# Kernel tuning notes

Measured on AMD Instinct MI355X. Metric: run time of the kernel, lower is better.

Reference implementation:

```python
import jax, jax.numpy as jnp
import numpy as np

SEARCH_RANGE = 4  # matches init_kwargs


def setup_inputs() -> dict:
    key = jax.random.key(0)
    k1, k2 = jax.random.split(key)
    shape = (8, 256, 64, 128)  # [B, C, H, W]
    feature1 = jax.random.normal(k1, shape, dtype=jnp.float32)
    feature2 = jax.random.normal(k2, shape, dtype=jnp.float32)
    return {"feature1": feature1, "feature2": feature2}


def reference(feature1, feature2):
    R = SEARCH_RANGE
    b, c, h, w = feature1.shape
    # zero-pad feature2 spatially by R on each side
    f2p = jnp.pad(feature2, ((0, 0), (0, 0), (R, R), (R, R)))
    D = 2 * R + 1
    # shift offsets in the same order as the original nested loop (idx outer, jdx inner)
    offsets = jnp.stack(
        jnp.meshgrid(jnp.arange(D), jnp.arange(D), indexing="ij"), axis=-1
    ).reshape(-1, 2)  # [81, 2]

    def corr_one(ij):
        win = jax.lax.dynamic_slice(f2p, (0, 0, ij[0], ij[1]), (b, c, h, w))
        return jnp.sum(feature1 * win, axis=1)  # [B, H, W]

    dots = jax.vmap(corr_one)(offsets)  # [81, B, H, W]
    return jnp.transpose(dots, (1, 0, 2, 3))  # [B, 81, H, W]
```

## Files before the change

kernel.cpp:

```cpp
#include <hip/hip_runtime.h>
#include <cstdint>

typedef __attribute__((ext_vector_type(8))) short short8;
typedef __attribute__((ext_vector_type(4))) float floatx4;
typedef __attribute__((ext_vector_type(2))) unsigned int uintx2;
typedef __attribute__((ext_vector_type(4))) unsigned int uintx4;

__device__ __forceinline__ uint32_t pack2(float a, float b) {
    uint32_t ua = __builtin_bit_cast(uint32_t, a);
    uint32_t ub = __builtin_bit_cast(uint32_t, b);
    ua = (ua + 0x7FFFu + ((ua >> 16) & 1u)) >> 16;
    ub = (ub + 0x7FFFu + ((ub >> 16) & 1u)) >> 16;
    return ua | (ub << 16);
}

#define CC_SLAB  ((size_t)8 * 64 * 2304)
#define T2P_WORDS (8 * CC_SLAB)
#define WS_NEED   (T2P_WORDS * 4 + 4096)

__global__ __launch_bounds__(256)
void transpose_f2(const float* __restrict__ f2, uint32_t* __restrict__ t2p) {
    __shared__ float t[64][33];
    const int tid = threadIdx.x;
    const int bid = blockIdx.x;
    const int b = bid & 7, h = (bid >> 3) & 63, wt = bid >> 9;
    const int w0 = wt * 32;
    const float* f2b = f2 + (size_t)b * 256 * 8192 + (size_t)h * 128 + w0;

    const int rw = tid & 31, rc8 = tid >> 5;
    const int tp = tid & 127, rr = tid >> 7;
    const int m  = tp & 15;

    for (int cc = 0; cc < 4; ++cc) {
        if (cc) __syncthreads();
#pragma unroll
        for (int i = 0; i < 8; ++i)
            t[rc8 * 8 + i][rw] = f2b[(size_t)(cc * 64 + rc8 * 8 + i) * 8192 + rw];
        __syncthreads();
        const int cc2 = 2 * cc + rr;
        uint32_t* dst = t2p + (size_t)cc2 * CC_SLAB
                        + ((size_t)b * 64 + h) * 2304 + (size_t)(w0 + 4) * 16;
#pragma unroll
        for (int i = 0; i < 4; ++i) {
            int d = i * 128 + tp;
            int j = d >> 4;
            dst[d] = pack2(t[rr * 32 + 2 * m][j], t[rr * 32 + 2 * m + 1][j]);
        }
    }
    if (wt == 0) {
        for (int idx = tid; idx < 512; idx += 256) {
            int cc2 = idx >> 6, o = idx & 63;
            t2p[(size_t)cc2 * CC_SLAB + ((size_t)b * 64 + h) * 2304 + o] = 0;
        }
    }
    if (wt == 3) {
        for (int idx = tid; idx < 1536; idx += 256) {
            int cc2 = idx / 192, o = idx % 192;
            t2p[(size_t)cc2 * CC_SLAB + ((size_t)b * 64 + h) * 2304 + 132 * 16 + o] = 0;
        }
    }
    if (bid == 0) {
        uint32_t* z = t2p + T2P_WORDS;
        for (int idx = tid; idx < 1024; idx += 256) z[idx] = 0;
    }
}

#define AS1 __attribute__((address_space(1)))
#define AS3 __attribute__((address_space(3)))

__device__ __forceinline__ void gld_lds16(const uint32_t* src, uint32_t* dst) {
    __builtin_amdgcn_global_load_lds((const AS1 void*)src, (AS3 void*)dst, 16, 0, 0);
}

__global__ __launch_bounds__(512, 3)
void corr2(const float* __restrict__ f1, const uint32_t* __restrict__ t2p,
           const uint32_t* __restrict__ wsZ, float* __restrict__ out) {
    __shared__ uint32_t ldsB[2 * 8192];

    const int tid  = threadIdx.x;
    const int lane = tid & 63;
    const int wh   = tid >> 6;
    const int n15  = lane & 15;
    const int q    = lane >> 4;

    const int bid = blockIdx.x;
    const int b  = bid & 7;
    const int ht = (bid >> 3) & 7;
    const int wt = bid >> 6;
    const int h0 = 8 * ht, w0 = 16 * wt;
    const int h  = h0 + wh;

    const float* f1b = f1 + (size_t)b * 256 * 8192;

    const uint32_t* bbase[4];
    size_t bstep[4];
    int bdst[4];
#pragma unroll
    for (int ki = 0; ki < 4; ++ki) {
        int k = 4 * wh + ki, r = k >> 1, gh = h0 - 4 + r;
        int c = (k & 1) * 16 + (lane >> 2);
        int gd = (lane & 3) ^ ((c >> 1) & 3);
        bool ok = (unsigned)gh < 64u;
        bbase[ki] = ok ? t2p + ((size_t)b * 64 + gh) * 2304 + (size_t)(w0 + c) * 16 + gd * 4
                       : wsZ + lane * 4;
        bstep[ki] = ok ? CC_SLAB : 0;
        bdst[ki]  = k * 256;
    }

    const float* aBase = f1b + (size_t)h * 128 + w0 + n15;

    floatx4 acc[9][2];
#pragma unroll
    for (int di = 0; di < 9; ++di)
#pragma unroll
        for (int t = 0; t < 2; ++t)
            acc[di][t] = (floatx4){0.f, 0.f, 0.f, 0.f};

    const int rdB = n15 * 16 + ((q ^ ((n15 >> 1) & 3)) << 2);

    auto stageB = [&](int bufsel, int cc) {
        uint32_t* dst = ldsB + bufsel * 8192;
#pragma unroll
        for (int ki = 0; ki < 4; ++ki)
            gld_lds16(bbase[ki] + (size_t)cc * bstep[ki], &dst[bdst[ki]]);
    };
    auto loadA = [&](float* r, int cc) {
        const float* ap = aBase + (size_t)(32 * cc + 8 * q) * 8192;
#pragma unroll
        for (int j = 0; j < 8; ++j) r[j] = ap[(size_t)j * 8192];
    };
    auto packA = [&](const float* r) -> short8 {
        uintx4 av = {pack2(r[0], r[1]), pack2(r[2], r[3]),
                     pack2(r[4], r[5]), pack2(r[6], r[7])};
        return __builtin_bit_cast(short8, av);
    };
    auto mfma9 = [&](int bufsel, short8 a0) {
        const uint32_t* bufB = ldsB + bufsel * 8192;
#pragma unroll
        for (int di = 0; di < 9; ++di) {
            const uint32_t* p0 = bufB + (wh + di) * 512 + rdB;
            uintx4 v0 = *(const uintx4*)p0;
            uintx4 v1 = *(const uintx4*)(p0 + 128);
            short8 b0 = __builtin_bit_cast(short8, v0);
            short8 b1 = __builtin_bit_cast(short8, v1);
            acc[di][0] = __builtin_amdgcn_mfma_f32_16x16x32_bf16(a0, b0, acc[di][0], 0, 0, 0);
            acc[di][1] = __builtin_amdgcn_mfma_f32_16x16x32_bf16(a0, b1, acc[di][1], 0, 0, 0);
        }
    };

    float rA0[8], rA1[8];

    stageB(0, 0);
    __builtin_amdgcn_sched_barrier(0);
    loadA(rA0, 0);
    __builtin_amdgcn_sched_barrier(0);
    stageB(1, 1);
    __builtin_amdgcn_sched_barrier(0);
    loadA(rA1, 1);
    __builtin_amdgcn_sched_barrier(0);

#define CHUNK(K, VM, RS)                                                      \
    {                                                                         \
        asm volatile("s_waitcnt vmcnt(" #VM ")\n\ts_barrier" ::: "memory");   \
        if ((K) >= 1 && (K) < 7) stageB(((K) + 1) & 1, (K) + 1);              \
        __builtin_amdgcn_sched_barrier(0);                                    \
        short8 a0 = packA(RS);                                                \
        if ((K) < 6) loadA(RS, (K) + 2);                                      \
        __builtin_amdgcn_sched_barrier(0);                                    \
        mfma9((K) & 1, a0);                                                   \
    }

    CHUNK(0, 20, rA0)
    CHUNK(1, 16, rA1)
    CHUNK(2, 8,  rA0)
    CHUNK(3, 8,  rA1)
    CHUNK(4, 8,  rA0)
    CHUNK(5, 8,  rA1)
    CHUNK(6, 8,  rA0)
    CHUNK(7, 0,  rA1)
#undef CHUNK

    const size_t base = ((size_t)b * 81) * 8192 + (size_t)h * 128 + w0;
#pragma unroll
    for (int di = 0; di < 9; ++di) {
#pragma unroll
        for (int t = 0; t < 2; ++t) {
#pragma unroll
            for (int r = 0; r < 4; ++r) {
                int mp = 4 * q + r;
                int dj = t * 8 + n15 - mp;
                if (dj >= 0 && dj <= 8 && (t == 0 || n15 >= 8)) {
                    out[base + (size_t)(di * 9 + dj) * 8192 + mp] = acc[di][t][r];
                }
            }
        }
    }
}

#define CS 18
#define A_WORDS (8 * 16 * CS)
#define B_ROWS  13
#define B_WORDS (B_ROWS * 24 * CS)

__device__ __forceinline__ short8 frag_ld(const uint32_t* p) {
    uintx2 lo = *(const uintx2*)p;
    uintx2 hi = *(const uintx2*)(p + 2);
    uintx4 v = {lo.x, lo.y, hi.x, hi.y};
    return __builtin_bit_cast(short8, v);
}

__global__ __launch_bounds__(512, 4)
void corr_kernel(const float* __restrict__ f1, const float* __restrict__ f2,
                 float* __restrict__ out) {
    __shared__ uint32_t ldsA[2 * A_WORDS];
    __shared__ uint32_t ldsB2[2 * B_WORDS];

    const int tid  = threadIdx.x;
    const int lane = tid & 63;
    const int wh   = tid >> 6;
    const int n15  = lane & 15;
    const int q    = lane >> 4;

    const int bid    = blockIdx.x;
    const int b      = bid & 7;
    const int dihalf = (bid >> 3) & 1;
    const int ht     = (bid >> 4) & 7;
    const int wt     = bid >> 7;

    const int w0 = wt * 16;
    const int h0 = ht * 8;
    const int h  = h0 + wh;

    const int diN    = dihalf ? 4 : 5;
    const int diBase = dihalf * 5;
    const int ghBase = dihalf ? (h0 + 1) : (h0 - 4);

    const float* f1b = f1 + (size_t)b * 256 * 8192;
    const float* f2b = f2 + (size_t)b * 256 * 8192;

    const int aw4 = tid & 3, akp = (tid >> 2) & 15, arow = tid >> 6;
    int aOffG = (2 * akp) * 8192 + (h0 + arow) * 128 + (w0 + 4 * aw4);
    const int aLds = (arow * 16 + 4 * aw4) * CS + akp;

    int bOffG[3]; int bLds[3]; uint32_t bMask[3];
#pragma unroll
    for (int s = 0; s < 3; ++s) {
        int t = tid + 512 * s;
        int w4 = t % 6;
        int r2 = t / 6;
        int kp = r2 & 15, row = r2 >> 4;
        int gh = ghBase + row;
        int gw = w0 - 4 + 4 * w4;
        bool live = (t < 1152);
        bool inb  = live && ((unsigned)gh < 64u) && ((unsigned)gw < 128u);
        bOffG[s] = inb ? ((2 * kp) * 8192 + gh * 128 + gw) : 0;
        bLds[s]  = live ? ((row * 24 + 4 * w4) * CS + kp) : ((12 * 24 + (tid & 7)) * CS);
        bMask[s] = inb ? 0xFFFFFFFFu : 0u;
    }

    floatx4 acc[5][2];
#pragma unroll
    for (int dl = 0; dl < 5; ++dl)
#pragma unroll
        for (int t = 0; t < 2; ++t)
            acc[dl][t] = (floatx4){0.f, 0.f, 0.f, 0.f};

    floatx4 rA[2], rB[3][2];
    uint32_t pkA[4], pkB[12];

    auto issue = [&]() {
        rA[0] = *(const floatx4*)(f1b + aOffG);
        rA[1] = *(const floatx4*)(f1b + aOffG + 8192);
        aOffG += 32 * 8192;
#pragma unroll
        for (int s = 0; s < 3; ++s) {
            rB[s][0] = *(const floatx4*)(f2b + bOffG[s]);
            rB[s][1] = *(const floatx4*)(f2b + bOffG[s] + 8192);
            bOffG[s] += 32 * 8192;
        }
    };
    auto packall = [&]() {
#pragma unroll
        for (int i = 0; i < 4; ++i) pkA[i] = pack2(rA[0][i], rA[1][i]);
#pragma unroll
        for (int s = 0; s < 3; ++s)
#pragma unroll
            for (int i = 0; i < 4; ++i)
                pkB[4 * s + i] = pack2(rB[s][0][i], rB[s][1][i]) & bMask[s];
    };

    issue(); packall();

    for (int ch = 0; ch < 8; ++ch) {
        uint32_t* bufA = ldsA + (ch & 1) * A_WORDS;
        uint32_t* bufB = ldsB2 + (ch & 1) * B_WORDS;
#pragma unroll
        for (int i = 0; i < 4; ++i) bufA[aLds + i * CS] = pkA[i];
#pragma unroll
        for (int s = 0; s < 3; ++s)
#pragma unroll
            for (int i = 0; i < 4; ++i) bufB[bLds[s] + i * CS] = pkB[4 * s + i];
        if (ch < 7) issue();
        __syncthreads();

        const uint32_t* pa = bufA + (wh * 16 + n15) * CS + 4 * q;
        short8 a0 = frag_ld(pa);
        const uint32_t* pb = bufB + (wh * 24 + n15) * CS + 4 * q;
#pragma unroll
        for (int dl = 0; dl < 5; ++dl) {
            if (dl < diN) {
                const uint32_t* pp = pb + dl * (24 * CS);
                short8 b0 = frag_ld(pp);
                short8 b1 = frag_ld(pp + 8 * CS);
                acc[dl][0] = __builtin_amdgcn_mfma_f32_16x16x32_bf16(a0, b0, acc[dl][0], 0, 0, 0);
                acc[dl][1] = __builtin_amdgcn_mfma_f32_16x16x32_bf16(a0, b1, acc[dl][1], 0, 0, 0);
            }
        }
        if (ch < 7) packall();
    }

    const size_t base = ((size_t)b * 81) * 8192 + (size_t)h * 128 + w0;
#pragma unroll
    for (int dl = 0; dl < 5; ++dl) {
        if (dl < diN) {
            const int dio = diBase + dl;
#pragma unroll
            for (int t = 0; t < 2; ++t) {
#pragma unroll
                for (int r = 0; r < 4; ++r) {
                    int mp = 4 * q + r;
                    int dj = t * 8 + n15 - mp;
                    if (dj >= 0 && dj <= 8 && (t == 0 || n15 >= 8)) {
                        out[base + (size_t)(dio * 9 + dj) * 8192 + mp] = acc[dl][t][r];
                    }
                }
            }
        }
    }
}

extern "C" void kernel_launch(void* const* d_in, const int* in_sizes, int n_in,
                              void* d_out, int out_size, void* d_ws, size_t ws_size,
                              hipStream_t stream) {
    const float* f1 = (const float*)d_in[0];
    const float* f2 = (const float*)d_in[1];
    float* out = (float*)d_out;
    if (ws_size >= WS_NEED && d_ws != nullptr) {
        uint32_t* t2p = (uint32_t*)d_ws;
        transpose_f2<<<dim3(2048), dim3(256), 0, stream>>>(f2, t2p);
        corr2<<<dim3(512), dim3(512), 0, stream>>>(f1, t2p, t2p + T2P_WORDS, out);
    } else {
        corr_kernel<<<dim3(1024), dim3(512), 0, stream>>>(f1, f2, out);
    }
}
```

Measured before the change: 177.3 us.

## Enlarge correlation tile to 16 rows with 1024-thread blocks and 4-stage B pipeline

The correlation kernel now uses 1024-thread blocks covering 16 output rows instead of 8, so each staged feature2 halo (24 rows) serves twice as many rows and less halo is reloaded. B staging grows from double to quadruple buffering, with dummy lanes dumping into a scratch LDS area. The channel-chunk order is rotated per block to spread memory traffic. The trade-off is fewer blocks (256), higher LDS use and a less uniform load mapping, which may reduce occupancy and latency hiding.

```diff
diff --git a/kernel.cpp b/kernel.cpp
--- a/kernel.cpp
+++ b/kernel.cpp
@@ -72,10 +72,13 @@
     __builtin_amdgcn_global_load_lds((const AS1 void*)src, (AS3 void*)dst, 16, 0, 0);
 }
 
-__global__ __launch_bounds__(512, 3)
-void corr2(const float* __restrict__ f1, const uint32_t* __restrict__ t2p,
+#define BUF_WORDS 9216
+#define DUMP_OFF  (4 * BUF_WORDS)
+
+__global__ __launch_bounds__(1024, 4)
+void corr3(const float* __restrict__ f1, const uint32_t* __restrict__ t2p,
            const uint32_t* __restrict__ wsZ, float* __restrict__ out) {
-    __shared__ uint32_t ldsB[2 * 8192];
+    __shared__ uint32_t ldsB[4 * BUF_WORDS + 256];
 
     const int tid  = threadIdx.x;
     const int lane = tid & 63;
@@ -85,26 +88,32 @@
 
     const int bid = blockIdx.x;
     const int b  = bid & 7;
-    const int ht = (bid >> 3) & 7;
-    const int wt = bid >> 6;
-    const int h0 = 8 * ht, w0 = 16 * wt;
+    const int ht = (bid >> 3) & 3;
+    const int wt = bid >> 5;
+    const int h0 = 16 * ht, w0 = 16 * wt;
     const int h  = h0 + wh;
+    const int p  = (ht + wt) & 7;
 
     const float* f1b = f1 + (size_t)b * 256 * 8192;
 
-    const uint32_t* bbase[4];
-    size_t bstep[4];
-    int bdst[4];
-#pragma unroll
-    for (int ki = 0; ki < 4; ++ki) {
-        int k = 4 * wh + ki, r = k >> 1, gh = h0 - 4 + r;
-        int c = (k & 1) * 16 + (lane >> 2);
-        int gd = (lane & 3) ^ ((c >> 1) & 3);
-        bool ok = (unsigned)gh < 64u;
-        bbase[ki] = ok ? t2p + ((size_t)b * 64 + gh) * 2304 + (size_t)(w0 + c) * 16 + gd * 4
-                       : wsZ + lane * 4;
-        bstep[ki] = ok ? CC_SLAB : 0;
-        bdst[ki]  = k * 256;
+    uint32_t bOff[3], ccMul[3];
+    int bOffL[3];
+    bool dumpf[3];
+#pragma unroll
+    for (int s = 0; s < 3; ++s) {
+        int sg = wh * 3 + s;
+        bool dummy = (sg & 3) == 3;
+        int rank = (sg >> 2) * 3 + (sg & 3);
+        int f = rank * 16 + (lane >> 2);
+        int r = f / 24, cidx = f % 24;
+        int gh = h0 - 4 + r;
+        int gd = (lane & 3) ^ ((cidx >> 1) & 3);
+        bool inb = !dummy && ((unsigned)gh < 64u);
+        bOff[s]  = inb ? (uint32_t)((b * 64 + gh) * 2304 + (w0 + cidx) * 16 + gd * 4)
+                       : (uint32_t)(T2P_WORDS + lane * 4);
+        ccMul[s] = inb ? (uint32_t)CC_SLAB : 0u;
+        bOffL[s] = rank * 256;
+        dumpf[s] = dummy;
     }
 
     const float* aBase = f1b + (size_t)h * 128 + w0 + n15;
@@ -119,10 +128,13 @@
     const int rdB = n15 * 16 + ((q ^ ((n15 >> 1) & 3)) << 2);
 
     auto stageB = [&](int bufsel, int cc) {
-        uint32_t* dst = ldsB + bufsel * 8192;
-#pragma unroll
-        for (int ki = 0; ki < 4; ++ki)
-            gld_lds16(bbase[ki] + (size_t)cc * bstep[ki], &dst[bdst[ki]]);
+        uint32_t* dbase = ldsB + bufsel * BUF_WORDS;
+#pragma unroll
+        for (int s = 0; s < 3; ++s) {
+            const uint32_t* src = t2p + (size_t)(bOff[s] + (uint32_t)cc * ccMul[s]);
+            uint32_t* d = dumpf[s] ? (ldsB + DUMP_OFF) : (dbase + bOffL[s]);
+            gld_lds16(src, d);
+        }
     };
     auto loadA = [&](float* r, int cc) {
         const float* ap = aBase + (size_t)(32 * cc + 8 * q) * 8192;
@@ -135,10 +147,10 @@
         return __builtin_bit_cast(short8, av);
     };
     auto mfma9 = [&](int bufsel, short8 a0) {
-        const uint32_t* bufB = ldsB + bufsel * 8192;
+        const uint32_t* bufB = ldsB + bufsel * BUF_WORDS;
 #pragma unroll
         for (int di = 0; di < 9; ++di) {
-            const uint32_t* p0 = bufB + (wh + di) * 512 + rdB;
+            const uint32_t* p0 = bufB + (wh + di) * 384 + rdB;
             uintx4 v0 = *(const uintx4*)p0;
             uintx4 v1 = *(const uintx4*)(p0 + 128);
             short8 b0 = __builtin_bit_cast(short8, v0);
@@ -149,36 +161,38 @@
     };
 
     float rA0[8], rA1[8];
-
-    stageB(0, 0);
-    __builtin_amdgcn_sched_barrier(0);
-    loadA(rA0, 0);
-    __builtin_amdgcn_sched_barrier(0);
-    stageB(1, 1);
-    __builtin_amdgcn_sched_barrier(0);
-    loadA(rA1, 1);
-    __builtin_amdgcn_sched_barrier(0);
+#define ROT(t) (((t) + p) & 7)
+#define SB __builtin_amdgcn_sched_barrier(0)
+
+    loadA(rA0, ROT(0)); SB;
+    stageB(0, ROT(0)); SB;
+    loadA(rA1, ROT(1)); SB;
+    stageB(1, ROT(1)); SB;
+    stageB(2, ROT(2)); SB;
 
 #define CHUNK(K, VM, RS)                                                      \
     {                                                                         \
         asm volatile("s_waitcnt vmcnt(" #VM ")\n\ts_barrier" ::: "memory");   \
-        if ((K) >= 1 && (K) < 7) stageB(((K) + 1) & 1, (K) + 1);              \
-        __builtin_amdgcn_sched_barrier(0);                                    \
         short8 a0 = packA(RS);                                                \
-        if ((K) < 6) loadA(RS, (K) + 2);                                      \
-        __builtin_amdgcn_sched_barrier(0);                                    \
-        mfma9((K) & 1, a0);                                                   \
-    }
-
-    CHUNK(0, 20, rA0)
-    CHUNK(1, 16, rA1)
-    CHUNK(2, 8,  rA0)
-    CHUNK(3, 8,  rA1)
-    CHUNK(4, 8,  rA0)
-    CHUNK(5, 8,  rA1)
-    CHUNK(6, 8,  rA0)
+        SB;                                                                   \
+        if ((K) <= 5) loadA(RS, ROT((K) + 2));                                \
+        SB;                                                                   \
+        if ((K) <= 4) stageB(((K) + 3) & 3, ROT((K) + 3));                    \
+        SB;                                                                   \
+        mfma9((K) & 3, a0);                                                   \
+    }
+
+    CHUNK(0, 14, rA0)
+    CHUNK(1, 14, rA1)
+    CHUNK(2, 14, rA0)
+    CHUNK(3, 14, rA1)
+    CHUNK(4, 14, rA0)
+    CHUNK(5, 14, rA1)
+    CHUNK(6, 11, rA0)
     CHUNK(7, 0,  rA1)
 #undef CHUNK
+#undef ROT
+#undef SB
 
     const size_t base = ((size_t)b * 81) * 8192 + (size_t)h * 128 + w0;
 #pragma unroll
@@ -348,7 +362,7 @@
     if (ws_size >= WS_NEED && d_ws != nullptr) {
         uint32_t* t2p = (uint32_t*)d_ws;
         transpose_f2<<<dim3(2048), dim3(256), 0, stream>>>(f2, t2p);
-        corr2<<<dim3(512), dim3(512), 0, stream>>>(f1, t2p, t2p + T2P_WORDS, out);
+        corr3<<<dim3(256), dim3(1024), 0, stream>>>(f1, t2p, t2p + T2P_WORDS, out);
     } else {
         corr_kernel<<<dim3(1024), dim3(512), 0, stream>>>(f1, f2, out);
     }
```

Result: slower. 181.8 us (+2.5%).
